# Performance work log

Hardware: AMD Instinct MI355X
Metric: run time of the kernel (lower is better)

Reference implementation:

```python
import jax, jax.numpy as jnp
import numpy as np

EPS = 1e-6

def _rmsnorm(x, w):
    # matches RMSNorm: compute in fp32, cast back, then scale by weight
    dt = x.dtype
    xf = x.astype(jnp.float32)
    var = jnp.mean(xf * xf, axis=-1, keepdims=True)
    xf = xf * jax.lax.rsqrt(var + EPS)
    return xf.astype(dt) * w


def setup_inputs() -> dict:
    key = jax.random.key(0)
    ks = jax.random.split(key, 4)
    B, N, C = 4, 2048, 1024
    H = 16
    D = C // H
    x = jax.random.normal(ks[0], (B, N, C), dtype=jnp.float32)
    W_qkv = jax.random.normal(ks[1], (C, 3 * C), dtype=jnp.float32) * (1.0 / np.sqrt(C))
    b_qkv = jnp.zeros((3 * C,), dtype=jnp.float32)
    W_proj = jax.random.normal(ks[2], (C, C), dtype=jnp.float32) * (1.0 / np.sqrt(C))
    b_proj = jnp.zeros((C,), dtype=jnp.float32)
    qn_w = jnp.ones((D,), dtype=jnp.float32)
    kn_w = jnp.ones((D,), dtype=jnp.float32)
    return {"x": x, "W_qkv": W_qkv, "b_qkv": b_qkv, "W_proj": W_proj,
            "b_proj": b_proj, "qn_w": qn_w, "kn_w": kn_w}


def reference(x, W_qkv, b_qkv, W_proj, b_proj, qn_w, kn_w):
    B, N, C = x.shape
    H = 16
    D = C // H
    qkv = jnp.einsum('bnc,cd->bnd', x, W_qkv) + b_qkv          # [B,N,3C]
    qkv = qkv.reshape(B, N, 3, H, D)
    q = qkv[:, :, 0].transpose(0, 2, 1, 3)                     # [B,H,N,D]
    k = qkv[:, :, 1].transpose(0, 2, 1, 3)
    v = qkv[:, :, 2].transpose(0, 2, 1, 3)
    q = _rmsnorm(q, qn_w)
    k = _rmsnorm(k, kn_w)
    scale = D ** -0.5
    attn = jnp.einsum('bhqd,bhkd->bhqk', q, k) * scale         # [B,H,N,N]
    attn = jax.nn.softmax(attn, axis=-1)
    out = jnp.einsum('bhqk,bhkd->bhqd', attn, v)               # [B,H,N,D]
    out = out.transpose(0, 2, 1, 3).reshape(B, N, C)
    out = jnp.einsum('bnc,cd->bnd', out, W_proj) + b_proj
    return out
```

## Files before the change

kernel.cpp:

```cpp
#include <hip/hip_runtime.h>
#include <stdint.h>

#define B_ 4
#define N_ 2048
#define C_ 1024
#define H_ 16
#define D_ 64
#define M_ (B_*N_)
#define N3_ (3*C_)

typedef __attribute__((ext_vector_type(8))) __bf16 bf16x8;
typedef bf16x8 bf16x8_ma __attribute__((may_alias));
typedef __attribute__((ext_vector_type(4))) float floatx4;
typedef unsigned short u16;
typedef unsigned int u32;

typedef __attribute__((address_space(1))) const void void_g;
typedef __attribute__((address_space(3))) void void_l;

__device__ __forceinline__ void glds16(const void* g, void* l) {
  __builtin_amdgcn_global_load_lds((void_g*)g, (void_l*)l, 16, 0, 0);
}

__device__ __forceinline__ u16 f2bf(float f) {
  union { float f; u32 u; } x; x.f = f;
  u32 r = x.u + 0x7fffu + ((x.u >> 16) & 1u);
  return (u16)(r >> 16);
}

__device__ __forceinline__ float fexp2(float x) {
#if __has_builtin(__builtin_amdgcn_exp2f)
  return __builtin_amdgcn_exp2f(x);
#else
  return exp2f(x);
#endif
}

__device__ __forceinline__ int xcd_swz(int hw, int nwg) {
  int per = nwg >> 3;
  return (hw & 7) * per + (hw >> 3);
}

__global__ __launch_bounds__(256)
void convert_x(const float4* __restrict__ in, uint2* __restrict__ out, int n4) {
  int idx = blockIdx.x * 256 + threadIdx.x;
  if (idx >= n4) return;
  float4 v = in[idx];
  union { u16 a[4]; uint2 u; } p;
  p.a[0] = f2bf(v.x); p.a[1] = f2bf(v.y); p.a[2] = f2bf(v.z); p.a[3] = f2bf(v.w);
  out[idx] = p.u;
}

__global__ __launch_bounds__(256)
void transpose_cvt(const float* __restrict__ in, u16* __restrict__ out,
                   int R, int Ccols) {
  __shared__ u16 tile[64][65];
  int c0 = blockIdx.x * 64, r0 = blockIdx.y * 64;
  int tid = threadIdx.x;
#pragma unroll
  for (int it = 0; it < 16; ++it) {
    int idx = it * 256 + tid;
    int r = idx >> 6, c = idx & 63;
    tile[c][r] = f2bf(in[(size_t)(r0 + r) * Ccols + c0 + c]);
  }
  __syncthreads();
#pragma unroll
  for (int it = 0; it < 16; ++it) {
    int idx = it * 256 + tid;
    int oc = idx >> 6, orr = idx & 63;
    out[(size_t)(c0 + oc) * R + r0 + orr] = tile[oc][orr];
  }
}

__global__ __launch_bounds__(256)
void transpose_v(const u16* __restrict__ qkv, u16* __restrict__ vt) {
  __shared__ u16 tile[64][65];
  int bh = blockIdx.y, b = bh >> 4, h = bh & 15;
  int n0 = blockIdx.x * 64;
  int tid = threadIdx.x;
#pragma unroll
  for (int it = 0; it < 16; ++it) {
    int idx = it * 256 + tid;
    int n = idx >> 6, d = idx & 63;
    tile[d][n] = qkv[(size_t)(b * N_ + n0 + n) * N3_ + 2 * C_ + h * D_ + d];
  }
  __syncthreads();
#pragma unroll
  for (int it = 0; it < 16; ++it) {
    int idx = it * 256 + tid;
    int d = idx >> 6, n = idx & 63;
    int np = (n & 0x23) | ((n & 0x0C) << 1) | ((n & 0x10) >> 2);
    vt[(size_t)(bh * D_ + d) * N_ + n0 + np] = tile[d][n];
  }
}

__global__ __launch_bounds__(512)
void gemm_qkv(const u16* __restrict__ A, const u16* __restrict__ Bt,
              const float* __restrict__ bias, u16* __restrict__ Cout,
              const float* __restrict__ qn, const float* __restrict__ kn) {
  __shared__ __align__(16) u16 sA[3][8 * 512];
  __shared__ __align__(16) u16 sB[3][16 * 512];
  const int K = C_;
  int tid = threadIdx.x;
  int wave = tid >> 6, lane = tid & 63;
  int lrow = lane & 15, lq = lane >> 4;
  int n0 = blockIdx.x * 256;
  int m0 = blockIdx.y * 128;
  int wm = wave >> 2, wn = wave & 3;

  floatx4 acc[4][4];
#pragma unroll
  for (int i = 0; i < 4; ++i)
#pragma unroll
    for (int j = 0; j < 4; ++j) acc[i][j] = (floatx4){0.f, 0.f, 0.f, 0.f};

  const u16* ga  = A  + (size_t)(m0 + wave * 16 + lrow) * K + lq * 8;
  const u16* gb0 = Bt + (size_t)(n0 + (2 * wave + 0) * 16 + lrow) * K + lq * 8;
  const u16* gb1 = Bt + (size_t)(n0 + (2 * wave + 1) * 16 + lrow) * K + lq * 8;
  int oa  = wave * 512;
  int ob0 = (2 * wave + 0) * 512;
  int ob1 = (2 * wave + 1) * 512;

#define STAGE(kt_, s_)                      \
  do {                                      \
    glds16(ga  + (kt_), &sA[s_][oa]);       \
    glds16(gb0 + (kt_), &sB[s_][ob0]);      \
    glds16(gb1 + (kt_), &sB[s_][ob1]);      \
  } while (0)

  STAGE(0, 0);
  STAGE(32, 1);

  int slot = 0;
  for (int kt = 0; kt < K; kt += 32) {
    if (kt + 32 < K) {
      asm volatile("s_waitcnt vmcnt(3)" ::: "memory");
    } else {
      asm volatile("s_waitcnt vmcnt(0)" ::: "memory");
    }
    __builtin_amdgcn_s_barrier();
    asm volatile("" ::: "memory");

    if (kt + 64 < K) {
      int s2 = slot + 2; if (s2 >= 3) s2 -= 3;
      STAGE(kt + 64, s2);
    }

    bf16x8 af[4], bfr[4];
#pragma unroll
    for (int i = 0; i < 4; ++i)
      af[i] = *(const bf16x8_ma*)(&sA[slot][(wm * 4 + i) * 512 + lane * 8]);
#pragma unroll
    for (int j = 0; j < 4; ++j)
      bfr[j] = *(const bf16x8_ma*)(&sB[slot][(wn * 4 + j) * 512 + lane * 8]);
#pragma unroll
    for (int i = 0; i < 4; ++i)
#pragma unroll
      for (int j = 0; j < 4; ++j)
        acc[i][j] = __builtin_amdgcn_mfma_f32_16x16x32_bf16(af[i], bfr[j], acc[i][j], 0, 0, 0);

    ++slot; if (slot >= 3) slot = 0;
  }
#undef STAGE

  int colbase = n0 + wn * 64;
  float bv[4];
#pragma unroll
  for (int j = 0; j < 4; ++j) bv[j] = bias[colbase + j * 16 + lrow];
#pragma unroll
  for (int i = 0; i < 4; ++i)
#pragma unroll
    for (int j = 0; j < 4; ++j)
#pragma unroll
      for (int r = 0; r < 4; ++r) acc[i][j][r] += bv[j];

  int sect = colbase >> 10;
  if (sect < 2) {
    const float* wptr = (sect == 0) ? qn : kn;
    float wv[4];
#pragma unroll
    for (int j = 0; j < 4; ++j) wv[j] = wptr[j * 16 + lrow];
#pragma unroll
    for (int i = 0; i < 4; ++i)
#pragma unroll
      for (int r = 0; r < 4; ++r) {
        float ss = 0.f;
#pragma unroll
        for (int j = 0; j < 4; ++j) { float v = acc[i][j][r]; ss += v * v; }
        ss += __shfl_xor(ss, 1);
        ss += __shfl_xor(ss, 2);
        ss += __shfl_xor(ss, 4);
        ss += __shfl_xor(ss, 8);
        float rstd = rsqrtf(ss * (1.0f / 64.0f) + 1e-6f);
#pragma unroll
        for (int j = 0; j < 4; ++j) acc[i][j][r] *= rstd * wv[j];
      }
  }

#pragma unroll
  for (int i = 0; i < 4; ++i)
#pragma unroll
    for (int j = 0; j < 4; ++j)
#pragma unroll
      for (int r = 0; r < 4; ++r) {
        int row = m0 + wm * 64 + i * 16 + lq * 4 + r;
        int col = colbase + j * 16 + lrow;
        Cout[(size_t)row * N3_ + col] = f2bf(acc[i][j][r]);
      }
}

__global__ __launch_bounds__(256)
void gemm_bt(const u16* __restrict__ A, const u16* __restrict__ Bt,
             const float* __restrict__ bias, void* __restrict__ Cout,
             int Ncols, int lda, int do_rms, int out_fp32,
             const float* __restrict__ qn, const float* __restrict__ kn) {
  __shared__ __align__(16) u16 sA[3][8 * 512];
  __shared__ __align__(16) u16 sB[3][8 * 512];
  const int K = C_;
  int tid = threadIdx.x;
  int wave = tid >> 6, lane = tid & 63;
  int lrow = lane & 15, lq = lane >> 4;

  int nwg = gridDim.x * gridDim.y;
  int hw = blockIdx.y * gridDim.x + blockIdx.x;
  int lg = xcd_swz(hw, nwg);
  int bx = lg % gridDim.x, by = lg / gridDim.x;
  int n0 = bx * 128;
  int m0 = by * 128;
  int wm = wave >> 1, wn = wave & 1;

  floatx4 acc[4][4];
#pragma unroll
  for (int i = 0; i < 4; ++i)
#pragma unroll
    for (int j = 0; j < 4; ++j) acc[i][j] = (floatx4){0.f, 0.f, 0.f, 0.f};

  const u16* ga0 = A  + (size_t)(m0 + (2 * wave + 0) * 16 + lrow) * lda + lq * 8;
  const u16* ga1 = A  + (size_t)(m0 + (2 * wave + 1) * 16 + lrow) * lda + lq * 8;
  const u16* gb0 = Bt + (size_t)(n0 + (2 * wave + 0) * 16 + lrow) * K + lq * 8;
  const u16* gb1 = Bt + (size_t)(n0 + (2 * wave + 1) * 16 + lrow) * K + lq * 8;
  int o0 = (2 * wave + 0) * 512;
  int o1 = (2 * wave + 1) * 512;

  u16* aA = &sA[0][0]; u16* aB = &sA[1][0]; u16* aC = &sA[2][0];
  u16* bA = &sB[0][0]; u16* bB = &sB[1][0]; u16* bC = &sB[2][0];

  glds16(ga0, aA + o0); glds16(ga1, aA + o1);
  glds16(gb0, bA + o0); glds16(gb1, bA + o1);
  glds16(ga0 + 32, aB + o0); glds16(ga1 + 32, aB + o1);
  glds16(gb0 + 32, bB + o0); glds16(gb1 + 32, bB + o1);

  for (int kt = 0; kt < K; kt += 32) {
    if (kt + 32 < K) {
      asm volatile("s_waitcnt vmcnt(4)" ::: "memory");
    } else {
      asm volatile("s_waitcnt vmcnt(0)" ::: "memory");
    }
    __builtin_amdgcn_s_barrier();
    asm volatile("" ::: "memory");

    if (kt + 64 < K) {
      glds16(ga0 + kt + 64, aC + o0);
      glds16(ga1 + kt + 64, aC + o1);
      glds16(gb0 + kt + 64, bC + o0);
      glds16(gb1 + kt + 64, bC + o1);
    }

    bf16x8 af[4], bfr[4];
#pragma unroll
    for (int i = 0; i < 4; ++i)
      af[i] = *(const bf16x8_ma*)(aA + (wm * 4 + i) * 512 + lane * 8);
#pragma unroll
    for (int j = 0; j < 4; ++j)
      bfr[j] = *(const bf16x8_ma*)(bA + (wn * 4 + j) * 512 + lane * 8);
#pragma unroll
    for (int i = 0; i < 4; ++i)
#pragma unroll
      for (int j = 0; j < 4; ++j)
        acc[i][j] = __builtin_amdgcn_mfma_f32_16x16x32_bf16(af[i], bfr[j], acc[i][j], 0, 0, 0);

    u16* t;
    t = aA; aA = aB; aB = aC; aC = t;
    t = bA; bA = bB; bB = bC; bC = t;
  }

  int colbase = n0 + wn * 64;
  float bv[4];
#pragma unroll
  for (int j = 0; j < 4; ++j) bv[j] = bias[colbase + j * 16 + lrow];
#pragma unroll
  for (int i = 0; i < 4; ++i)
#pragma unroll
    for (int j = 0; j < 4; ++j)
#pragma unroll
      for (int r = 0; r < 4; ++r) acc[i][j][r] += bv[j];

  int sect = colbase >> 10;
  if (do_rms && sect < 2) {
    const float* wptr = (sect == 0) ? qn : kn;
    float wv[4];
#pragma unroll
    for (int j = 0; j < 4; ++j) wv[j] = wptr[j * 16 + lrow];
#pragma unroll
    for (int i = 0; i < 4; ++i)
#pragma unroll
      for (int r = 0; r < 4; ++r) {
        float ss = 0.f;
#pragma unroll
        for (int j = 0; j < 4; ++j) { float v = acc[i][j][r]; ss += v * v; }
        ss += __shfl_xor(ss, 1);
        ss += __shfl_xor(ss, 2);
        ss += __shfl_xor(ss, 4);
        ss += __shfl_xor(ss, 8);
        float rstd = rsqrtf(ss * (1.0f / 64.0f) + 1e-6f);
#pragma unroll
        for (int j = 0; j < 4; ++j) acc[i][j][r] *= rstd * wv[j];
      }
  }

#pragma unroll
  for (int i = 0; i < 4; ++i)
#pragma unroll
    for (int j = 0; j < 4; ++j)
#pragma unroll
      for (int r = 0; r < 4; ++r) {
        int row = m0 + wm * 64 + i * 16 + lq * 4 + r;
        int col = colbase + j * 16 + lrow;
        if (out_fp32)
          ((float*)Cout)[(size_t)row * Ncols + col] = acc[i][j][r];
        else
          ((u16*)Cout)[(size_t)row * Ncols + col] = f2bf(acc[i][j][r]);
      }
}

__global__ __launch_bounds__(512)
void flash_attn(u16* __restrict__ qkv, const u16* __restrict__ vt) {
  __shared__ __align__(16) u16 sK[2][8 * 512];
  __shared__ __align__(16) u16 sV[2][8 * 512];
  int tid = threadIdx.x;
  int wave = tid >> 6, lane = tid & 63;
  int lrow = lane & 15, lq = lane >> 4;

  int hw = blockIdx.y * gridDim.x + blockIdx.x;
  int lg = xcd_swz(hw, 512);
  int qblk = lg & 7, bh = lg >> 3;
  int b = bh >> 4, h = bh & 15;
  int q0 = qblk * 256;
  const float cc = 0.125f * 1.44269504088896340736f;

  bf16x8 qf[2][2];
#pragma unroll
  for (int i = 0; i < 2; ++i)
#pragma unroll
    for (int kq = 0; kq < 2; ++kq) {
      union { bf16x8 v; __bf16 e[8]; } t;
      t.v = *(const bf16x8_ma*)(qkv +
          (size_t)(b * N_ + q0 + wave * 32 + i * 16 + lrow) * N3_ +
          h * D_ + kq * 32 + lq * 8);
#pragma unroll
      for (int e = 0; e < 8; ++e) t.e[e] = (__bf16)((float)t.e[e] * cc);
      qf[i][kq] = t.v;
    }

  union { bf16x8 v; u16 e[8]; } one_;
#pragma unroll
  for (int e = 0; e < 8; ++e) one_.e[e] = 0x3F80;
  bf16x8 onef = one_.v;

  floatx4 aco[2][4];
  floatx4 acl[2];
#pragma unroll
  for (int i = 0; i < 2; ++i) {
#pragma unroll
    for (int nd = 0; nd < 4; ++nd) aco[i][nd] = (floatx4){0.f, 0.f, 0.f, 0.f};
    acl[i] = (floatx4){0.f, 0.f, 0.f, 0.f};
  }

  const u16* gk = qkv + (size_t)(b * N_ + (wave >> 1) * 16 + lrow) * N3_ +
                  C_ + h * D_ + (wave & 1) * 32 + lq * 8;
  const u16* gv = vt + (size_t)(bh * D_ + (wave >> 1) * 16 + lrow) * N_ +
                  (wave & 1) * 32 + lq * 8;

  u16* k_cur = &sK[0][0]; u16* k_nxt = &sK[1][0];
  u16* v_cur = &sV[0][0]; u16* v_nxt = &sV[1][0];

  glds16(gk, k_cur + wave * 512);
  glds16(gv, v_cur + wave * 512);
  __syncthreads();

  for (int kt = 0; kt < 32; ++kt) {
    if (kt < 31) {
      size_t key0n = (size_t)(kt + 1) * 64;
      glds16(gk + key0n * N3_, k_nxt + wave * 512);
      glds16(gv + key0n, v_nxt + wave * 512);
    }

    floatx4 accs[2][4];
    __builtin_amdgcn_s_setprio(1);
#pragma unroll
    for (int j = 0; j < 4; ++j) {
      bf16x8 kf0 = *(const bf16x8_ma*)(k_cur + (j * 2 + 0) * 512 + lane * 8);
      bf16x8 kf1 = *(const bf16x8_ma*)(k_cur + (j * 2 + 1) * 512 + lane * 8);
#pragma unroll
      for (int i = 0; i < 2; ++i) {
        floatx4 s = (floatx4){0.f, 0.f, 0.f, 0.f};
        s = __builtin_amdgcn_mfma_f32_16x16x32_bf16(kf0, qf[i][0], s, 0, 0, 0);
        s = __builtin_amdgcn_mfma_f32_16x16x32_bf16(kf1, qf[i][1], s, 0, 0, 0);
        accs[i][j] = s;
      }
    }
    __builtin_amdgcn_s_setprio(0);

    bf16x8 pf[2][2];
#pragma unroll
    for (int i = 0; i < 2; ++i) {
      union { bf16x8 v; __bf16 e[8]; } pk0, pk1;
#pragma unroll
      for (int j = 0; j < 4; ++j)
#pragma unroll
        for (int r = 0; r < 4; ++r) {
          float p = fexp2(accs[i][j][r]);
          if (j < 2) pk0.e[(j & 1) * 4 + r] = (__bf16)p;
          else       pk1.e[(j & 1) * 4 + r] = (__bf16)p;
        }
      pf[i][0] = pk0.v;
      pf[i][1] = pk1.v;
    }

    __builtin_amdgcn_s_setprio(1);
#pragma unroll
    for (int kq = 0; kq < 2; ++kq) {
#pragma unroll
      for (int nd = 0; nd < 4; ++nd) {
        bf16x8 vf = *(const bf16x8_ma*)(v_cur + (nd * 2 + kq) * 512 + lane * 8);
        aco[0][nd] = __builtin_amdgcn_mfma_f32_16x16x32_bf16(vf, pf[0][kq], aco[0][nd], 0, 0, 0);
        aco[1][nd] = __builtin_amdgcn_mfma_f32_16x16x32_bf16(vf, pf[1][kq], aco[1][nd], 0, 0, 0);
      }
      acl[0] = __builtin_amdgcn_mfma_f32_16x16x32_bf16(onef, pf[0][kq], acl[0], 0, 0, 0);
      acl[1] = __builtin_amdgcn_mfma_f32_16x16x32_bf16(onef, pf[1][kq], acl[1], 0, 0, 0);
    }
    __builtin_amdgcn_s_setprio(0);

    __syncthreads();
    u16* t0 = k_cur; k_cur = k_nxt; k_nxt = t0;
    u16* t1 = v_cur; v_cur = v_nxt; v_nxt = t1;
  }

#pragma unroll
  for (int i = 0; i < 2; ++i) {
    float inv = 1.0f / acl[i][0];
    int row = q0 + wave * 32 + i * 16 + lrow;
#pragma unroll
    for (int nd = 0; nd < 4; ++nd) {
      union { u16 a[4]; uint2 u; } st;
#pragma unroll
      for (int r = 0; r < 4; ++r) st.a[r] = f2bf(aco[i][nd][r] * inv);
      *(uint2*)(qkv + (size_t)(b * N_ + row) * N3_ + h * D_ + nd * 16 + lq * 4) = st.u;
    }
  }
}

extern "C" void kernel_launch(void* const* d_in, const int* in_sizes, int n_in,
                              void* d_out, int out_size, void* d_ws, size_t ws_size,
                              hipStream_t stream) {
  (void)in_sizes; (void)n_in; (void)out_size; (void)ws_size;
  const float* x     = (const float*)d_in[0];
  const float* Wqkv  = (const float*)d_in[1];
  const float* bqkv  = (const float*)d_in[2];
  const float* Wproj = (const float*)d_in[3];
  const float* bproj = (const float*)d_in[4];
  const float* qn    = (const float*)d_in[5];
  const float* kn    = (const float*)d_in[6];
  float* out = (float*)d_out;

  char* ws = (char*)d_ws;
  u16* xb      = (u16*)ws;  ws += (size_t)M_ * C_ * 2;
  u16* Wt_qkv  = (u16*)ws;  ws += (size_t)N3_ * C_ * 2;
  u16* Wt_proj = (u16*)ws;  ws += (size_t)C_ * C_ * 2;
  u16* qkv     = (u16*)ws;  ws += (size_t)M_ * N3_ * 2;
  u16* vt      = (u16*)ws;  ws += (size_t)B_ * H_ * D_ * N_ * 2;

  convert_x<<<dim3(M_ * C_ / 4 / 256), 256, 0, stream>>>(
      (const float4*)x, (uint2*)xb, M_ * C_ / 4);
  transpose_cvt<<<dim3(N3_ / 64, C_ / 64), 256, 0, stream>>>(Wqkv, Wt_qkv, C_, N3_);
  transpose_cvt<<<dim3(C_ / 64, C_ / 64), 256, 0, stream>>>(Wproj, Wt_proj, C_, C_);
  gemm_qkv<<<dim3(N3_ / 256, M_ / 128), 512, 0, stream>>>(
      xb, Wt_qkv, bqkv, qkv, qn, kn);
  transpose_v<<<dim3(N_ / 64, B_ * H_), 256, 0, stream>>>(qkv, vt);
  flash_attn<<<dim3(N_ / 256, B_ * H_), 512, 0, stream>>>(qkv, vt);
  gemm_bt<<<dim3(C_ / 128, M_ / 128), 256, 0, stream>>>(
      qkv, Wt_proj, bproj, out, C_, N3_, 0, 1, qn, kn);
}
```

Measured before the change: 300.1 us.

## Fuse prep kernels into one launch; load QKV GEMM operands directly from global

Merges the x conversion and both weight transpose-conversions into a single prep kernel that dispatches on block id, saving two launches. The QKV GEMM drops its LDS triple-buffer pipeline and instead loads MFMA fragments straight from global memory (relying on L2) with register double buffering. Tiles shrink to 128x128 with 256 threads. It removes LDS staging and barriers but risks uncoalesced and redundant global loads, since operands are no longer shared across waves.

```diff
diff --git a/kernel.cpp b/kernel.cpp
--- a/kernel.cpp
+++ b/kernel.cpp
@@ -42,21 +42,32 @@
 }
 
 __global__ __launch_bounds__(256)
-void convert_x(const float4* __restrict__ in, uint2* __restrict__ out, int n4) {
-  int idx = blockIdx.x * 256 + threadIdx.x;
-  if (idx >= n4) return;
-  float4 v = in[idx];
-  union { u16 a[4]; uint2 u; } p;
-  p.a[0] = f2bf(v.x); p.a[1] = f2bf(v.y); p.a[2] = f2bf(v.z); p.a[3] = f2bf(v.w);
-  out[idx] = p.u;
-}
-
-__global__ __launch_bounds__(256)
-void transpose_cvt(const float* __restrict__ in, u16* __restrict__ out,
-                   int R, int Ccols) {
+void prep(const float4* __restrict__ x4, uint2* __restrict__ xb,
+          const float* __restrict__ Wqkv, u16* __restrict__ Wt_qkv,
+          const float* __restrict__ Wproj, u16* __restrict__ Wt_proj) {
   __shared__ u16 tile[64][65];
-  int c0 = blockIdx.x * 64, r0 = blockIdx.y * 64;
+  int id = blockIdx.x;
   int tid = threadIdx.x;
+
+  if (id < 8192) {
+    int idx = id * 256 + tid;
+    float4 v = x4[idx];
+    union { u16 a[4]; uint2 u; } p;
+    p.a[0] = f2bf(v.x); p.a[1] = f2bf(v.y); p.a[2] = f2bf(v.z); p.a[3] = f2bf(v.w);
+    xb[idx] = p.u;
+    return;
+  }
+
+  const float* in; u16* out; int R, Ccols, c0, r0;
+  if (id < 8192 + 768) {
+    int lid = id - 8192;
+    in = Wqkv; out = Wt_qkv; R = C_; Ccols = N3_;
+    c0 = (lid % 48) * 64; r0 = (lid / 48) * 64;
+  } else {
+    int lid = id - 8960;
+    in = Wproj; out = Wt_proj; R = C_; Ccols = C_;
+    c0 = (lid & 15) * 64; r0 = (lid >> 4) * 64;
+  }
 #pragma unroll
   for (int it = 0; it < 16; ++it) {
     int idx = it * 256 + tid;
@@ -94,19 +105,17 @@
   }
 }
 
-__global__ __launch_bounds__(512)
-void gemm_qkv(const u16* __restrict__ A, const u16* __restrict__ Bt,
-              const float* __restrict__ bias, u16* __restrict__ Cout,
-              const float* __restrict__ qn, const float* __restrict__ kn) {
-  __shared__ __align__(16) u16 sA[3][8 * 512];
-  __shared__ __align__(16) u16 sB[3][16 * 512];
+__global__ __launch_bounds__(256)
+void gemm_qkv_l2(const u16* __restrict__ A, const u16* __restrict__ Bt,
+                 const float* __restrict__ bias, u16* __restrict__ Cout,
+                 const float* __restrict__ qn, const float* __restrict__ kn) {
   const int K = C_;
   int tid = threadIdx.x;
   int wave = tid >> 6, lane = tid & 63;
   int lrow = lane & 15, lq = lane >> 4;
-  int n0 = blockIdx.x * 256;
+  int n0 = blockIdx.x * 128;
   int m0 = blockIdx.y * 128;
-  int wm = wave >> 2, wn = wave & 3;
+  int wm = wave >> 1, wn = wave & 1;
 
   floatx4 acc[4][4];
 #pragma unroll
@@ -114,54 +123,46 @@
 #pragma unroll
     for (int j = 0; j < 4; ++j) acc[i][j] = (floatx4){0.f, 0.f, 0.f, 0.f};
 
-  const u16* ga  = A  + (size_t)(m0 + wave * 16 + lrow) * K + lq * 8;
-  const u16* gb0 = Bt + (size_t)(n0 + (2 * wave + 0) * 16 + lrow) * K + lq * 8;
-  const u16* gb1 = Bt + (size_t)(n0 + (2 * wave + 1) * 16 + lrow) * K + lq * 8;
-  int oa  = wave * 512;
-  int ob0 = (2 * wave + 0) * 512;
-  int ob1 = (2 * wave + 1) * 512;
-
-#define STAGE(kt_, s_)                      \
-  do {                                      \
-    glds16(ga  + (kt_), &sA[s_][oa]);       \
-    glds16(gb0 + (kt_), &sB[s_][ob0]);      \
-    glds16(gb1 + (kt_), &sB[s_][ob1]);      \
-  } while (0)
-
-  STAGE(0, 0);
-  STAGE(32, 1);
-
-  int slot = 0;
-  for (int kt = 0; kt < K; kt += 32) {
-    if (kt + 32 < K) {
-      asm volatile("s_waitcnt vmcnt(3)" ::: "memory");
-    } else {
-      asm volatile("s_waitcnt vmcnt(0)" ::: "memory");
-    }
-    __builtin_amdgcn_s_barrier();
-    asm volatile("" ::: "memory");
+  const u16* pa[4];
+  const u16* pb[4];
+#pragma unroll
+  for (int i = 0; i < 4; ++i) {
+    pa[i] = A  + (size_t)(m0 + wm * 64 + i * 16 + lrow) * K + lq * 8;
+    pb[i] = Bt + (size_t)(n0 + wn * 64 + i * 16 + lrow) * K + lq * 8;
+  }
+
+  bf16x8 a0[4], b0[4], a1[4], b1[4];
+#pragma unroll
+  for (int i = 0; i < 4; ++i) {
+    a0[i] = *(const bf16x8_ma*)(pa[i]);
+    b0[i] = *(const bf16x8_ma*)(pb[i]);
+  }
+
+  for (int kt = 0; kt < K; kt += 64) {
+#pragma unroll
+    for (int i = 0; i < 4; ++i) {
+      a1[i] = *(const bf16x8_ma*)(pa[i] + kt + 32);
+      b1[i] = *(const bf16x8_ma*)(pb[i] + kt + 32);
+    }
+#pragma unroll
+    for (int i = 0; i < 4; ++i)
+#pragma unroll
+      for (int j = 0; j < 4; ++j)
+        acc[i][j] = __builtin_amdgcn_mfma_f32_16x16x32_bf16(a0[i], b0[j], acc[i][j], 0, 0, 0);
 
     if (kt + 64 < K) {
-      int s2 = slot + 2; if (s2 >= 3) s2 -= 3;
-      STAGE(kt + 64, s2);
-    }
-
-    bf16x8 af[4], bfr[4];
-#pragma unroll
-    for (int i = 0; i < 4; ++i)
-      af[i] = *(const bf16x8_ma*)(&sA[slot][(wm * 4 + i) * 512 + lane * 8]);
-#pragma unroll
-    for (int j = 0; j < 4; ++j)
-      bfr[j] = *(const bf16x8_ma*)(&sB[slot][(wn * 4 + j) * 512 + lane * 8]);
+#pragma unroll
+      for (int i = 0; i < 4; ++i) {
+        a0[i] = *(const bf16x8_ma*)(pa[i] + kt + 64);
+        b0[i] = *(const bf16x8_ma*)(pb[i] + kt + 64);
+      }
+    }
 #pragma unroll
     for (int i = 0; i < 4; ++i)
 #pragma unroll
       for (int j = 0; j < 4; ++j)
-        acc[i][j] = __builtin_amdgcn_mfma_f32_16x16x32_bf16(af[i], bfr[j], acc[i][j], 0, 0, 0);
-
-    ++slot; if (slot >= 3) slot = 0;
-  }
-#undef STAGE
+        acc[i][j] = __builtin_amdgcn_mfma_f32_16x16x32_bf16(a1[i], b1[j], acc[i][j], 0, 0, 0);
+  }
 
   int colbase = n0 + wn * 64;
   float bv[4];
@@ -480,11 +481,9 @@
   u16* qkv     = (u16*)ws;  ws += (size_t)M_ * N3_ * 2;
   u16* vt      = (u16*)ws;  ws += (size_t)B_ * H_ * D_ * N_ * 2;
 
-  convert_x<<<dim3(M_ * C_ / 4 / 256), 256, 0, stream>>>(
-      (const float4*)x, (uint2*)xb, M_ * C_ / 4);
-  transpose_cvt<<<dim3(N3_ / 64, C_ / 64), 256, 0, stream>>>(Wqkv, Wt_qkv, C_, N3_);
-  transpose_cvt<<<dim3(C_ / 64, C_ / 64), 256, 0, stream>>>(Wproj, Wt_proj, C_, C_);
-  gemm_qkv<<<dim3(N3_ / 256, M_ / 128), 512, 0, stream>>>(
+  prep<<<dim3(8192 + 768 + 256), 256, 0, stream>>>(
+      (const float4*)x, (uint2*)xb, Wqkv, Wt_qkv, Wproj, Wt_proj);
+  gemm_qkv_l2<<<dim3(N3_ / 128, M_ / 128), 256, 0, stream>>>(
       xb, Wt_qkv, bqkv, qkv, qn, kn);
   transpose_v<<<dim3(N_ / 64, B_ * H_), 256, 0, stream>>>(qkv, vt);
   flash_attn<<<dim3(N_ / 256, B_ * H_), 512, 0, stream>>>(qkv, vt);
```

Measured after the change: 387.4 us. 1.29x slower.
